# Performance work log

Measured on AMD Instinct MI355X. Metric: run time of the kernel, lower is better.

## Reference

```python
import jax, jax.numpy as jnp
import numpy as np

B, S, D = 4, 1024, 768
H = 12
E = 4
DF = 3072
TOPK = 2
# expert domain map: language->0 (LINGUISTIC), logic->1 (SYMBOLIC), spatial->0, causal->1
DOMAIN_MAP = jnp.array([0, 1, 0, 1], dtype=jnp.int32)


def layernorm(x, g, b, eps=1e-5):
    mu = jnp.mean(x, axis=-1, keepdims=True)
    var = jnp.mean(jnp.square(x - mu), axis=-1, keepdims=True)
    return (x - mu) * jax.lax.rsqrt(var + eps) * g + b


def setup_inputs() -> dict:
    key = jax.random.key(0)
    ks = jax.random.split(key, 10)
    sc = 0.02
    return {
        "x": jax.random.normal(ks[0], (B, S, D), jnp.float32),
        "ln1_g": jnp.ones((D,), jnp.float32),
        "ln1_b": jnp.zeros((D,), jnp.float32),
        "Wq": jax.random.normal(ks[1], (D, D), jnp.float32) * sc,
        "Wk": jax.random.normal(ks[2], (D, D), jnp.float32) * sc,
        "Wv": jax.random.normal(ks[3], (D, D), jnp.float32) * sc,
        "Wo": jax.random.normal(ks[4], (D, D), jnp.float32) * sc,
        "Wt": jax.random.normal(ks[5], (D, 2), jnp.float32) * sc,
        "bt": jnp.zeros((2,), jnp.float32),
        "ln2_g": jnp.ones((D,), jnp.float32),
        "ln2_b": jnp.zeros((D,), jnp.float32),
        "Wg": jax.random.normal(ks[6], (D, E), jnp.float32) * sc,
        "W1": jax.random.normal(ks[7], (E, D, DF), jnp.float32) * sc,
        "b1": jnp.zeros((E, DF), jnp.float32),
        "W2": jax.random.normal(ks[8], (E, DF, D), jnp.float32) * sc,
        "b2": jnp.zeros((E, D), jnp.float32),
    }


def reference(x, ln1_g, ln1_b, Wq, Wk, Wv, Wo, Wt, bt, ln2_g, ln2_b, Wg, W1, b1, W2, b2):
    hd = D // H
    # --- task-conditioned routing bias ---
    pooled = jnp.mean(x, axis=1)                      # [B, D]
    task_logits = pooled @ Wt + bt                    # [B, 2]
    routing_bias = task_logits[:, DOMAIN_MAP]         # [B, E]
    # --- multi-head self-attention with pre-norm residual ---
    h = layernorm(x, ln1_g, ln1_b)
    q = (h @ Wq).reshape(B, S, H, hd)
    k = (h @ Wk).reshape(B, S, H, hd)
    v = (h @ Wv).reshape(B, S, H, hd)
    scores = jnp.einsum("bqhd,bkhd->bhqk", q, k) / jnp.sqrt(jnp.float32(hd))
    attn = jax.nn.softmax(scores, axis=-1)
    ctx = jnp.einsum("bhqk,bkhd->bqhd", attn, v).reshape(B, S, D)
    x = x + ctx @ Wo
    # --- top-k MoE with routing bias, pre-norm residual ---
    h2 = layernorm(x, ln2_g, ln2_b)
    gate_logits = h2 @ Wg + routing_bias[:, None, :]  # [B, S, E]
    topv, topi = jax.lax.top_k(gate_logits, TOPK)     # [B, S, k]
    w = jax.nn.softmax(topv, axis=-1)                 # renormalized top-k weights
    gates = jnp.sum(jax.nn.one_hot(topi, E, dtype=x.dtype) * w[..., None], axis=-2)  # [B,S,E]
    hid = jax.nn.gelu(jnp.einsum("bsd,edf->bsef", h2, W1) + b1)       # [B,S,E,DF]
    y = jnp.einsum("bsef,efd->bsed", hid, W2) + b2                    # [B,S,E,D]
    moe_out = jnp.einsum("bsed,bse->bsd", y, gates)
    return x + moe_out
```

## Files before the change

kernel.cpp:

```cpp
#include <hip/hip_runtime.h>
#include <hip/hip_bf16.h>

using bf16 = __hip_bfloat16;
typedef float f32x4 __attribute__((ext_vector_type(4)));
typedef short bf16x8 __attribute__((ext_vector_type(8)));

#define DD 768
#define SS 1024
#define HH 12
#define DFF 3072

__device__ __forceinline__ float bf2f(bf16 v) { return __bfloat162float(v); }
__device__ __forceinline__ bf16 f2bf(float v) { return __float2bfloat16(v); }
__device__ __forceinline__ float sb2f(short u) {
  return __uint_as_float(((unsigned)(unsigned short)u) << 16);
}
__device__ __forceinline__ short f2sb(float f) {
  bf16 b = f2bf(f);
  return reinterpret_cast<short&>(b);
}

__device__ __forceinline__ void gld16(const void* g, void* l) {
  __builtin_amdgcn_global_load_lds(
      (const __attribute__((address_space(1))) void*)g,
      (__attribute__((address_space(3))) void*)l, 16, 0, 0);
}

__global__ __launch_bounds__(256) void transpose_cast_kernel(
    const float* __restrict__ src, bf16* __restrict__ dst,
    int R, int C, long sstride, long dstride)
{
  __shared__ float tile[64][65];
  const int c0 = blockIdx.x * 64, r0 = blockIdx.y * 64;
  const float* s = src + (long)blockIdx.z * sstride + (long)r0 * C + c0;
  bf16* d = dst + (long)blockIdx.z * dstride + (long)c0 * R + r0;
  const int rr = threadIdx.x >> 4;
  const int cc = (threadIdx.x & 15) * 4;
  #pragma unroll
  for (int k = 0; k < 4; k++) {
    const f32x4 v = *(const f32x4*)(s + (long)(rr + k * 16) * C + cc);
    *(f32x4*)(&tile[rr + k * 16][cc]) = v;
  }
  __syncthreads();
  #pragma unroll
  for (int k = 0; k < 4; k++) {
    const int c = rr + k * 16;
    short4 pk = make_short4(f2sb(tile[cc + 0][c]), f2sb(tile[cc + 1][c]),
                            f2sb(tile[cc + 2][c]), f2sb(tile[cc + 3][c]));
    *(short4*)(d + (long)c * R + cc) = pk;
  }
}

__global__ __launch_bounds__(256) void transpose4_kernel(
    const float* __restrict__ s0, const float* __restrict__ s1,
    const float* __restrict__ s2, const float* __restrict__ s3,
    bf16* __restrict__ dst)
{
  __shared__ float tile[64][65];
  const int z = blockIdx.z;
  const float* src = (z == 0) ? s0 : (z == 1) ? s1 : (z == 2) ? s2 : s3;
  const int c0 = blockIdx.x * 64, r0 = blockIdx.y * 64;
  const float* s = src + (long)r0 * 768 + c0;
  bf16* d = dst + (long)z * 589824 + (long)c0 * 768 + r0;
  const int rr = threadIdx.x >> 4;
  const int cc = (threadIdx.x & 15) * 4;
  #pragma unroll
  for (int k = 0; k < 4; k++) {
    const f32x4 v = *(const f32x4*)(s + (long)(rr + k * 16) * 768 + cc);
    *(f32x4*)(&tile[rr + k * 16][cc]) = v;
  }
  __syncthreads();
  #pragma unroll
  for (int k = 0; k < 4; k++) {
    const int c = rr + k * 16;
    short4 pk = make_short4(f2sb(tile[cc + 0][c]), f2sb(tile[cc + 1][c]),
                            f2sb(tile[cc + 2][c]), f2sb(tile[cc + 3][c]));
    *(short4*)(d + (long)c * 768 + cc) = pk;
  }
}

__global__ __launch_bounds__(256) void ln1pool_kernel(
    const float* __restrict__ x, const float* __restrict__ g,
    const float* __restrict__ b, bf16* __restrict__ out,
    float* __restrict__ pp)
{
  __shared__ float buf[4][768];
  const int w = threadIdx.x >> 6, lane = threadIdx.x & 63;
  const int row = blockIdx.x * 4 + w;
  const float* xr = x + (long)row * DD;
  float v[12];
  float s = 0.f;
  #pragma unroll
  for (int i = 0; i < 12; i++) { v[i] = xr[lane + i * 64]; s += v[i]; }
  #pragma unroll
  for (int o = 1; o < 64; o <<= 1) s += __shfl_xor(s, o, 64);
  const float mu = s * (1.f / DD);
  float vs = 0.f;
  #pragma unroll
  for (int i = 0; i < 12; i++) { const float d = v[i] - mu; vs += d * d; }
  #pragma unroll
  for (int o = 1; o < 64; o <<= 1) vs += __shfl_xor(vs, o, 64);
  const float rstd = rsqrtf(vs * (1.f / DD) + 1e-5f);
  bf16* orow = out + (long)row * DD;
  #pragma unroll
  for (int i = 0; i < 12; i++) {
    const int d = lane + i * 64;
    orow[d] = f2bf((v[i] - mu) * rstd * g[d] + b[d]);
    buf[w][d] = v[i];
  }
  __syncthreads();
  for (int c = threadIdx.x; c < 768; c += 256)
    pp[(long)blockIdx.x * 768 + c] = buf[0][c] + buf[1][c] + buf[2][c] + buf[3][c];
}

__global__ __launch_bounds__(256) void pool2_kernel(
    const float* __restrict__ pp, float* __restrict__ pooled)
{
  const int idx = blockIdx.x * 256 + threadIdx.x;
  const int bb = idx / 768, d = idx % 768;
  const float* p = pp + (long)bb * 256 * 768 + d;
  float s = 0.f;
  for (int c = 0; c < 256; c++) s += p[(long)c * 768];
  pooled[idx] = s * (1.f / SS);
}

__global__ __launch_bounds__(256) void route_kernel(
    const float* __restrict__ pooled, const float* __restrict__ Wt,
    const float* __restrict__ bt, float* __restrict__ rbias)
{
  __shared__ float tl[8];
  const int pair = threadIdx.x >> 5, l = threadIdx.x & 31;
  const int b = pair >> 1, j = pair & 1;
  float s = 0.f;
  for (int i = l; i < DD; i += 32) s += pooled[b * DD + i] * Wt[i * 2 + j];
  #pragma unroll
  for (int o = 1; o < 32; o <<= 1) s += __shfl_xor(s, o, 64);
  if (l == 0) tl[pair] = s + bt[j];
  __syncthreads();
  if (threadIdx.x < 16) {
    const int bb = threadIdx.x >> 2, e = threadIdx.x & 3;
    rbias[threadIdx.x] = tl[bb * 2 + (e & 1)];
  }
}

__device__ __forceinline__ float gelu_tanh(float x) {
  const float u = 0.7978845608028654f * (x + 0.044715f * x * x * x);
  const float e = __expf(2.f * u);
  const float t = 1.f - 2.f / (e + 1.f);
  return 0.5f * x * (1.f + t);
}

template <int MODE>
__global__ __launch_bounds__(256) void gemm128_kernel(
    const bf16* __restrict__ A, const bf16* __restrict__ Bt,
    bf16* __restrict__ Cbf, float* __restrict__ Cf,
    int N, int K, int NT, int GX,
    const float* __restrict__ aux1)
{
  __shared__ __align__(16) bf16 As[2][128 * 32];
  __shared__ __align__(16) bf16 Bs[2][128 * 32];

  const int nwg = gridDim.x;
  const int orig = blockIdx.x;
  const int q = nwg >> 3, r = nwg & 7;
  const int xcd = orig & 7, sidx = orig >> 3;
  const int wgid = (xcd < r ? xcd * (q + 1) : r * (q + 1) + (xcd - r) * q) + sidx;

  const int n0 = (wgid % GX) * 128;
  const int m0 = (wgid / GX) * 128;

  const int tid = threadIdx.x;
  const int lane = tid & 63, wv = tid >> 6;
  const int wr = wv >> 1, wc = wv & 1;
  const int lrow = lane & 15, lk = lane >> 4;
  const int lr = lrow, lg = lk;
  const int srow = lane >> 2;
  const int csw = (((lane & 3) ^ ((srow >> 1) & 3)) * 8);

  const bf16* arow[2];
  const bf16* brow[2];
  #pragma unroll
  for (int u = 0; u < 2; u++) {
    const int rbr = u * 64 + wv * 16 + srow;
    arow[u] = A + (long)(m0 + rbr) * K;
    brow[u] = Bt + (long)(n0 + rbr) * K;
  }

  f32x4 acc[4][4] = {};

#define STAGE(T, BUF)                                                   \
  {                                                                     \
    const int k0s = (T) * 32;                                           \
    _Pragma("unroll")                                                   \
    for (int u = 0; u < 2; u++) {                                       \
      const int rb = u * 64 + wv * 16;                                  \
      gld16(arow[u] + k0s + csw, &As[BUF][rb * 32]);                    \
      gld16(brow[u] + k0s + csw, &Bs[BUF][rb * 32]);                    \
    }                                                                   \
  }

  STAGE(0, 0)
  __syncthreads();

  for (int t = 0; t < NT; t++) {
    const int buf = t & 1;
    if (t + 1 < NT) STAGE(t + 1, buf ^ 1)

    bf16x8 af[4], bfr[4];
    #pragma unroll
    for (int i = 0; i < 4; i++) {
      const int ra = wr * 64 + i * 16 + lrow;
      const int rbw = wc * 64 + i * 16 + lrow;
      af[i]  = *(const bf16x8*)(&As[buf][ra * 32 + ((lk ^ ((ra >> 1) & 3)) * 8)]);
      bfr[i] = *(const bf16x8*)(&Bs[buf][rbw * 32 + ((lk ^ ((rbw >> 1) & 3)) * 8)]);
    }
    #pragma unroll
    for (int i = 0; i < 4; i++)
      #pragma unroll
      for (int j = 0; j < 4; j++)
        acc[i][j] = __builtin_amdgcn_mfma_f32_16x16x32_bf16(bfr[j], af[i], acc[i][j], 0, 0, 0);
    __syncthreads();
  }
#undef STAGE

  #pragma unroll
  for (int i = 0; i < 4; i++) {
    const int rloc = wr * 64 + i * 16 + lr;
    #pragma unroll
    for (int j = 0; j < 4; j++) {
      const int col = n0 + wc * 64 + j * 16 + lg * 4;
      const f32x4 v = acc[i][j];
      if (MODE == 0) {
        const long row = m0 + rloc;
        short4 pk = make_short4(f2sb(v[0]), f2sb(v[1]), f2sb(v[2]), f2sb(v[3]));
        *(short4*)(&Cbf[row * N + col]) = pk;
      } else {
        const long idx = (long)(m0 + rloc) * N + col;
        const f32x4 xv = *(const f32x4*)(&aux1[idx]);
        f32x4 o = xv + v;
        *(f32x4*)(&Cf[idx]) = o;
      }
    }
  }
}

template <int MODE>
__global__ __launch_bounds__(512, 2) void gemm256s_kernel(
    const bf16* __restrict__ A, const bf16* __restrict__ Bt,
    bf16* __restrict__ Cbf,
    int N, int K, int NT, int GX,
    const float* __restrict__ aux1, const float* __restrict__ gates,
    const int* __restrict__ tokl, const int* __restrict__ cnt_es,
    bf16* __restrict__ yB)
{
  __shared__ __align__(16) bf16 As[2][256 * 32];
  __shared__ __align__(16) bf16 Bs[2][256 * 32];

  const int nwg = gridDim.x;
  const int orig = blockIdx.x;
  const int q = nwg >> 3, r = nwg & 7;
  const int xcd = orig & 7, sidx = orig >> 3;
  const int wgid = (xcd < r ? xcd * (q + 1) : r * (q + 1) + (xcd - r) * q) + sidx;

  const int n0 = (wgid % GX) * 256;
  int e = 0, g0 = 0, row0 = 0, nval = 0, kseg = 0, kh = 0;
  {
    int p = wgid / GX;
    if (MODE == 3) { kh = p & 1; p >>= 1; }
    int sacc = 0, pacc = 0, found = 0;
    #pragma unroll
    for (int k = 0; k < 8; k++) {
      const int c = cnt_es[k];
      const int pk = (c + 255) >> 8;
      if (!found && p < pacc + pk) {
        found = 1; kseg = k; e = k & 3;
        g0 = (p - pacc) * 256; row0 = sacc + g0; nval = c;
      }
      pacc += pk; sacc += c;
    }
    if (!found) return;
  }
  const int kofs = (MODE == 3) ? kh * 1536 : 0;

  const int tid = threadIdx.x;
  const int lane = tid & 63, wv = tid >> 6;
  const int wr = wv >> 2, wc = wv & 3;
  const int lrow = lane & 15, lk = lane >> 4;
  const int lr = lrow, lg = lk;
  const int srow = lane >> 2;
  const int csw = (((lane & 3) ^ ((srow >> 1) & 3)) * 8);

  const bf16* Be = Bt + (long)e * N * K;
  const bf16* arow[2];
  const bf16* brow[2];
  #pragma unroll
  for (int u = 0; u < 2; u++) {
    const int rbr = u * 128 + wv * 16 + srow;
    if (MODE == 2) {
      const int g = g0 + rbr;
      const int tk = (g < nval) ? tokl[kseg * 4096 + g] : tokl[kseg * 4096];
      arow[u] = A + (long)tk * K;
    } else {
      int rr = row0 + rbr; if (rr > 8191) rr = 8191;
      arow[u] = A + (long)rr * K + kofs;
    }
    brow[u] = Be + (long)(n0 + rbr) * K + kofs;
  }

  f32x4 acc[8][4] = {};

#define STAGE(T, BUF)                                                   \
  {                                                                     \
    const int k0s = (T) * 32;                                           \
    _Pragma("unroll")                                                   \
    for (int u = 0; u < 2; u++) {                                       \
      const int rb = u * 128 + wv * 16;                                 \
      gld16(arow[u] + k0s + csw, &As[BUF][rb * 32]);                    \
      gld16(brow[u] + k0s + csw, &Bs[BUF][rb * 32]);                    \
    }                                                                   \
  }

  STAGE(0, 0)
  __syncthreads();

  for (int t = 0; t < NT; t++) {
    const int buf = t & 1;
    if (t + 1 < NT) STAGE(t + 1, buf ^ 1)

    bf16x8 af[8], bfr[4];
    #pragma unroll
    for (int j = 0; j < 4; j++) {
      const int rbw = wc * 64 + j * 16 + lrow;
      bfr[j] = *(const bf16x8*)(&Bs[buf][rbw * 32 + ((lk ^ ((rbw >> 1) & 3)) * 8)]);
    }
    #pragma unroll
    for (int i = 0; i < 8; i++) {
      const int ra = wr * 128 + i * 16 + lrow;
      af[i] = *(const bf16x8*)(&As[buf][ra * 32 + ((lk ^ ((ra >> 1) & 3)) * 8)]);
    }
    #pragma unroll
    for (int i = 0; i < 8; i++)
      #pragma unroll
      for (int j = 0; j < 4; j++)
        acc[i][j] = __builtin_amdgcn_mfma_f32_16x16x32_bf16(bfr[j], af[i], acc[i][j], 0, 0, 0);
    __syncthreads();
  }
#undef STAGE

  #pragma unroll
  for (int i = 0; i < 8; i++) {
    const int g = g0 + wr * 128 + i * 16 + lr;
    if (g < nval) {
      #pragma unroll
      for (int j = 0; j < 4; j++) {
        const int col = n0 + wc * 64 + j * 16 + lg * 4;
        const f32x4 v = acc[i][j];
        if (MODE == 2) {
          const float* b1e = aux1 + (long)e * N;
          const f32x4 bb = *(const f32x4*)(&b1e[col]);
          short4 pk = make_short4(f2sb(gelu_tanh(v[0] + bb[0])),
                                  f2sb(gelu_tanh(v[1] + bb[1])),
                                  f2sb(gelu_tanh(v[2] + bb[2])),
                                  f2sb(gelu_tanh(v[3] + bb[3])));
          *(short4*)(&Cbf[(long)(row0 - g0 + g) * N + col]) = pk;
        } else {
          const int tk = tokl[kseg * 4096 + g];
          const float gt = gates[tk * 4 + e];
          f32x4 vb = v;
          if (kh == 0) {
            const float* b2e = aux1 + (long)e * N;
            const f32x4 bb = *(const f32x4*)(&b2e[col]);
            vb = v + bb;
          }
          const int pidx = (kseg >> 2) * 2 + kh;
          bf16* yp = (pidx < 3) ? Cbf + (long)pidx * 3145728 : yB;
          short4 pk = make_short4(f2sb(gt * vb[0]), f2sb(gt * vb[1]),
                                  f2sb(gt * vb[2]), f2sb(gt * vb[3]));
          *(short4*)(&yp[(long)tk * 768 + col]) = pk;
        }
      }
    }
  }
}

__global__ __launch_bounds__(256) void fuse_kernel(
    const bf16* __restrict__ yA, const bf16* __restrict__ yB,
    float* __restrict__ out)
{
  const long i = ((long)blockIdx.x * 256 + threadIdx.x) * 4;
  const short4 a = *(const short4*)((const short*)yA + i);
  const short4 b = *(const short4*)((const short*)yA + 3145728 + i);
  const short4 c = *(const short4*)((const short*)yA + 6291456 + i);
  const short4 d = *(const short4*)((const short*)yB + i);
  f32x4 o = *(f32x4*)(&out[i]);
  o[0] += sb2f(a.x) + sb2f(b.x) + sb2f(c.x) + sb2f(d.x);
  o[1] += sb2f(a.y) + sb2f(b.y) + sb2f(c.y) + sb2f(d.y);
  o[2] += sb2f(a.z) + sb2f(b.z) + sb2f(c.z) + sb2f(d.z);
  o[3] += sb2f(a.w) + sb2f(b.w) + sb2f(c.w) + sb2f(d.w);
  *(f32x4*)(&out[i]) = o;
}

__global__ __launch_bounds__(256) void vtrans_kernel(
    const bf16* __restrict__ qkv, bf16* __restrict__ vt)
{
  __shared__ short t[64][72];
  const int kt = blockIdx.x;
  const int bh = blockIdx.y;
  const int b = bh / HH, h = bh % HH;
  const int tid = threadIdx.x;
  const short* vg = (const short*)qkv + ((long)(b * SS + kt * 64)) * 2304 + 1536 + h * 64;
  #pragma unroll
  for (int i = 0; i < 2; i++) {
    const int idx = i * 256 + tid;
    const int r = idx >> 3, c = (idx & 7) * 8;
    *(bf16x8*)(&t[r][c]) = *(const bf16x8*)(vg + (long)r * 2304 + c);
  }
  __syncthreads();
  short* vo = (short*)vt + (long)bh * 64 * SS + kt * 64;
  #pragma unroll
  for (int i = 0; i < 2; i++) {
    const int idx = i * 256 + tid;
    const int d = idx >> 3, r0 = (idx & 7) * 8;
    bf16x8 o;
    #pragma unroll
    for (int j = 0; j < 8; j++) o[j] = t[r0 + j][d];
    *(bf16x8*)(vo + (long)d * SS + r0) = o;
  }
}

__global__ __launch_bounds__(256) void attn_kernel(
    const bf16* __restrict__ qkv, const bf16* __restrict__ vt,
    bf16* __restrict__ ctx)
{
  __shared__ __align__(16) short Qs[64 * 64];
  __shared__ __align__(16) short Ks[64 * 64];
  __shared__ __align__(16) short Vts[64 * 64];
  __shared__ __align__(16) short Ps[4][16 * 64];

  const int qt = blockIdx.x;
  const int bh = blockIdx.y;
  const int b = bh / HH, h = bh % HH;
  const int tid = threadIdx.x, lane = tid & 63, w = tid >> 6;
  const int lr = lane & 15, lg = lane >> 4;

  const short* qg = (const short*)qkv + ((long)(b * SS + qt * 64)) * 2304 + h * 64;
  #pragma unroll
  for (int i = 0; i < 2; i++) {
    const int idx = i * 256 + tid;
    const int r = idx >> 3, c8 = idx & 7;
    bf16x8 v = *(const bf16x8*)(qg + (long)r * 2304 + c8 * 8);
    bf16x8 o;
    #pragma unroll
    for (int j = 0; j < 8; j++) o[j] = f2sb(sb2f(v[j]) * 0.125f);
    *(bf16x8*)(&Qs[r * 64 + ((c8 ^ (r & 7)) * 8)]) = o;
  }
  __syncthreads();

  bf16x8 aq[2];
  {
    const int r = w * 16 + lr;
    aq[0] = *(const bf16x8*)(&Qs[r * 64 + (((lg + 0) ^ (r & 7)) * 8)]);
    aq[1] = *(const bf16x8*)(&Qs[r * 64 + (((lg + 4) ^ (r & 7)) * 8)]);
  }

  float m_run[4], l_run[4];
  f32x4 oacc[4];
  #pragma unroll
  for (int r = 0; r < 4; r++) { m_run[r] = -1e30f; l_run[r] = 0.f; }
  #pragma unroll
  for (int dt = 0; dt < 4; dt++) oacc[dt] = (f32x4){0.f, 0.f, 0.f, 0.f};

  const short* kg = (const short*)qkv + ((long)(b * SS)) * 2304 + 768 + h * 64;
  const short* vg = (const short*)vt + ((long)bh * 64) * SS;
  const int sr = lane >> 3, sc = lane & 7;

  for (int kt = 0; kt < 16; kt++) {
    __syncthreads();
    #pragma unroll
    for (int c = 0; c < 2; c++) {
      const int rb = c * 32 + w * 8;
      const int row = rb + sr;
      const int ch = sc ^ (row & 7);
      gld16(kg + ((long)(kt * 64 + row)) * 2304 + ch * 8, &Ks[rb * 64]);
      gld16(vg + ((long)row) * SS + kt * 64 + ch * 8, &Vts[rb * 64]);
    }
    __syncthreads();

    f32x4 s[4];
    #pragma unroll
    for (int jt = 0; jt < 4; jt++) {
      const int r = jt * 16 + lr;
      bf16x8 bk0 = *(const bf16x8*)(&Ks[r * 64 + (((lg + 0) ^ (r & 7)) * 8)]);
      bf16x8 bk1 = *(const bf16x8*)(&Ks[r * 64 + (((lg + 4) ^ (r & 7)) * 8)]);
      f32x4 a = {};
      a = __builtin_amdgcn_mfma_f32_16x16x32_bf16(aq[0], bk0, a, 0, 0, 0);
      a = __builtin_amdgcn_mfma_f32_16x16x32_bf16(aq[1], bk1, a, 0, 0, 0);
      s[jt] = a;
    }

    #pragma unroll
    for (int r = 0; r < 4; r++) {
      float mt = fmaxf(fmaxf(s[0][r], s[1][r]), fmaxf(s[2][r], s[3][r]));
      mt = fmaxf(mt, __shfl_xor(mt, 1, 64));
      mt = fmaxf(mt, __shfl_xor(mt, 2, 64));
      mt = fmaxf(mt, __shfl_xor(mt, 4, 64));
      mt = fmaxf(mt, __shfl_xor(mt, 8, 64));
      const float mn = fmaxf(m_run[r], mt);
      const float sc0 = __expf(m_run[r] - mn);
      m_run[r] = mn;
      float p0 = __expf(s[0][r] - mn), p1 = __expf(s[1][r] - mn);
      float p2 = __expf(s[2][r] - mn), p3 = __expf(s[3][r] - mn);
      float rs = p0 + p1 + p2 + p3;
      rs += __shfl_xor(rs, 1, 64);
      rs += __shfl_xor(rs, 2, 64);
      rs += __shfl_xor(rs, 4, 64);
      rs += __shfl_xor(rs, 8, 64);
      l_run[r] = l_run[r] * sc0 + rs;
      #pragma unroll
      for (int dt = 0; dt < 4; dt++) oacc[dt][r] *= sc0;
      const int prow = lg * 4 + r;
      const int pswz = (prow & 7) << 3;
      Ps[w][prow * 64 + ((0 * 16 + lr) ^ pswz)] = f2sb(p0);
      Ps[w][prow * 64 + ((1 * 16 + lr) ^ pswz)] = f2sb(p1);
      Ps[w][prow * 64 + ((2 * 16 + lr) ^ pswz)] = f2sb(p2);
      Ps[w][prow * 64 + ((3 * 16 + lr) ^ pswz)] = f2sb(p3);
    }

    bf16x8 pa0 = *(const bf16x8*)(&Ps[w][lr * 64 + (((lg + 0) ^ (lr & 7)) << 3)]);
    bf16x8 pa1 = *(const bf16x8*)(&Ps[w][lr * 64 + (((lg + 4) ^ (lr & 7)) << 3)]);
    #pragma unroll
    for (int dt = 0; dt < 4; dt++) {
      const int r = dt * 16 + lr;
      bf16x8 bv0 = *(const bf16x8*)(&Vts[r * 64 + (((lg + 0) ^ (r & 7)) * 8)]);
      bf16x8 bv1 = *(const bf16x8*)(&Vts[r * 64 + (((lg + 4) ^ (r & 7)) * 8)]);
      oacc[dt] = __builtin_amdgcn_mfma_f32_16x16x32_bf16(pa0, bv0, oacc[dt], 0, 0, 0);
      oacc[dt] = __builtin_amdgcn_mfma_f32_16x16x32_bf16(pa1, bv1, oacc[dt], 0, 0, 0);
    }
  }

  #pragma unroll
  for (int r = 0; r < 4; r++) {
    const float inv = 1.f / l_run[r];
    const long row = (long)(b * SS + qt * 64 + w * 16 + lg * 4 + r);
    #pragma unroll
    for (int dt = 0; dt < 4; dt++)
      ctx[row * DD + h * 64 + dt * 16 + lr] = f2bf(oacc[dt][r] * inv);
  }
}

__global__ __launch_bounds__(256) void lngate_kernel(
    const float* __restrict__ x2, const float* __restrict__ g,
    const float* __restrict__ bln, const float* __restrict__ Wg,
    const float* __restrict__ rbias, bf16* __restrict__ h2,
    float* __restrict__ gates)
{
  const int t = blockIdx.x * 4 + (threadIdx.x >> 6);
  const int lane = threadIdx.x & 63;
  const int b = t >> 10;
  const float* xr = x2 + (long)t * DD;
  float v[12];
  float s = 0.f;
  #pragma unroll
  for (int i = 0; i < 12; i++) { v[i] = xr[lane + i * 64]; s += v[i]; }
  #pragma unroll
  for (int o = 1; o < 64; o <<= 1) s += __shfl_xor(s, o, 64);
  const float mu = s * (1.f / DD);
  float vs = 0.f;
  #pragma unroll
  for (int i = 0; i < 12; i++) { const float d = v[i] - mu; vs += d * d; }
  #pragma unroll
  for (int o = 1; o < 64; o <<= 1) vs += __shfl_xor(vs, o, 64);
  const float rstd = rsqrtf(vs * (1.f / DD) + 1e-5f);
  bf16* orow = h2 + (long)t * DD;
  float a0 = 0.f, a1 = 0.f, a2 = 0.f, a3 = 0.f;
  #pragma unroll
  for (int i = 0; i < 12; i++) {
    const int d = lane + i * 64;
    const float hv = (v[i] - mu) * rstd * g[d] + bln[d];
    orow[d] = f2bf(hv);
    const f32x4 w = *(const f32x4*)(&Wg[d * 4]);
    a0 += hv * w.x; a1 += hv * w.y; a2 += hv * w.z; a3 += hv * w.w;
  }
  #pragma unroll
  for (int o = 1; o < 64; o <<= 1) {
    a0 += __shfl_xor(a0, o, 64); a1 += __shfl_xor(a1, o, 64);
    a2 += __shfl_xor(a2, o, 64); a3 += __shfl_xor(a3, o, 64);
  }
  if (lane == 0) {
    float lg4[4] = { a0 + rbias[b * 4 + 0], a1 + rbias[b * 4 + 1],
                     a2 + rbias[b * 4 + 2], a3 + rbias[b * 4 + 3] };
    int i1 = 0;
    #pragma unroll
    for (int e = 1; e < 4; e++) if (lg4[e] > lg4[i1]) i1 = e;
    int i2 = -1;
    #pragma unroll
    for (int e = 0; e < 4; e++) if (e != i1 && (i2 < 0 || lg4[e] > lg4[i2])) i2 = e;
    const float e2 = __expf(lg4[i2] - lg4[i1]);
    const float den = 1.f + e2;
    float og[4] = {0.f, 0.f, 0.f, 0.f};
    og[i1] = 1.f / den;
    og[i2] = e2 / den;
    *(f32x4*)(&gates[t * 4]) = (f32x4){og[0], og[1], og[2], og[3]};
  }
}

__global__ __launch_bounds__(1024) void compact_kernel(
    const float* __restrict__ gates, int* __restrict__ tokl,
    int* __restrict__ cnt)
{
  __shared__ int wtot[8][16];
  const int tid = threadIdx.x;
  const int lane = tid & 63, w = tid >> 6;
  int sA[4], sB[4];
  int lc[8] = {0, 0, 0, 0, 0, 0, 0, 0};
  #pragma unroll
  for (int i = 0; i < 4; i++) {
    const int t = tid * 4 + i;
    const f32x4 g = *(const f32x4*)(&gates[t * 4]);
    int e1 = -1, e2 = -1;
    #pragma unroll
    for (int e = 0; e < 4; e++)
      if (g[e] > 0.f) { if (e1 < 0) e1 = e; else e2 = e; }
    sA[i] = e1; sB[i] = 4 + e2;
    lc[e1]++; lc[4 + e2]++;
  }
  int base[8];
  #pragma unroll
  for (int k = 0; k < 8; k++) {
    int v = lc[k];
    #pragma unroll
    for (int o = 1; o < 64; o <<= 1) {
      const int u = __shfl_up(v, o, 64);
      if (lane >= o) v += u;
    }
    base[k] = v - lc[k];
    if (lane == 63) wtot[k][w] = v;
  }
  __syncthreads();
  #pragma unroll
  for (int k = 0; k < 8; k++) {
    int b = 0;
    for (int ww = 0; ww < 16; ww++)
      if (ww < w) b += wtot[k][ww];
    base[k] += b;
  }
  #pragma unroll
  for (int i = 0; i < 4; i++) {
    const int t = tid * 4 + i;
    tokl[sA[i] * 4096 + base[sA[i]]] = t; base[sA[i]]++;
    tokl[sB[i] * 4096 + base[sB[i]]] = t; base[sB[i]]++;
  }
  if (tid < 8) {
    int s = 0;
    for (int ww = 0; ww < 16; ww++) s += wtot[tid][ww];
    cnt[tid] = s;
  }
}

extern "C" void kernel_launch(void* const* d_in, const int* in_sizes, int n_in,
                              void* d_out, int out_size, void* d_ws, size_t ws_size,
                              hipStream_t stream)
{
  (void)in_sizes; (void)n_in; (void)out_size; (void)ws_size;
  const float* x    = (const float*)d_in[0];
  const float* ln1g = (const float*)d_in[1];
  const float* ln1b = (const float*)d_in[2];
  const float* Wq   = (const float*)d_in[3];
  const float* Wk   = (const float*)d_in[4];
  const float* Wv   = (const float*)d_in[5];
  const float* Wo   = (const float*)d_in[6];
  const float* Wt   = (const float*)d_in[7];
  const float* bt   = (const float*)d_in[8];
  const float* ln2g = (const float*)d_in[9];
  const float* ln2b = (const float*)d_in[10];
  const float* Wg   = (const float*)d_in[11];
  const float* W1   = (const float*)d_in[12];
  const float* b1   = (const float*)d_in[13];
  const float* W2   = (const float*)d_in[14];
  const float* b2   = (const float*)d_in[15];
  float* out = (float*)d_out;

  char* ws = (char*)d_ws;
  bf16*  w1t    = (bf16*)(ws + 0);
  bf16*  w2t    = (bf16*)(ws + 18874368);
  bf16*  h2     = (bf16*)(ws + 37748736);
  float* gates  = (float*)(ws + 44040192);
  int*   tokl   = (int*)(ws + 44105728);
  int*   cnt    = (int*)(ws + 44236800);
  float* pooled = (float*)(ws + 44237056);
  float* rbias  = (float*)(ws + 44249344);
  bf16*  wqkv_t = (bf16*)(ws + 44249600);
  bf16*  h1     = (bf16*)(ws + 48968192);
  bf16*  qkv    = (bf16*)(ws + 55259648);
  bf16*  ctx    = (bf16*)(ws + 74134016);
  bf16*  hid    = (bf16*)(ws + 44249600);
  bf16*  wo_t   = wqkv_t + 3 * 589824;
  bf16*  vt     = h1;
  bf16*  yA     = w1t;
  bf16*  yB     = h2;
  float* pp     = (float*)qkv;

  transpose4_kernel<<<dim3(12, 12, 4), 256, 0, stream>>>(Wq, Wk, Wv, Wo, wqkv_t);
  transpose_cast_kernel<<<dim3(48, 12, 4), 256, 0, stream>>>(W1, w1t, 768, 3072, 2359296, 2359296);
  transpose_cast_kernel<<<dim3(12, 48, 4), 256, 0, stream>>>(W2, w2t, 3072, 768, 2359296, 2359296);

  ln1pool_kernel<<<1024, 256, 0, stream>>>(x, ln1g, ln1b, h1, pp);
  pool2_kernel<<<12, 256, 0, stream>>>(pp, pooled);
  route_kernel<<<1, 256, 0, stream>>>(pooled, Wt, bt, rbias);

  gemm128_kernel<0><<<32 * 18, 256, 0, stream>>>(h1, wqkv_t, qkv, nullptr,
                                                 2304, 768, 24, 18, nullptr);
  vtrans_kernel<<<dim3(16, 48), 256, 0, stream>>>(qkv, vt);
  attn_kernel<<<dim3(16, 48), 256, 0, stream>>>(qkv, vt, ctx);
  gemm128_kernel<1><<<32 * 6, 256, 0, stream>>>(ctx, wo_t, nullptr, out,
                                                768, 768, 24, 6, x);
  lngate_kernel<<<1024, 256, 0, stream>>>(out, ln2g, ln2b, Wg, rbias, h2, gates);
  compact_kernel<<<1, 1024, 0, stream>>>(gates, tokl, cnt);

  gemm256s_kernel<2><<<40 * 12, 512, 0, stream>>>(h2, w1t, hid,
                                                  3072, 768, 24, 12,
                                                  b1, nullptr, tokl, cnt, nullptr);
  gemm256s_kernel<3><<<40 * 2 * 3, 512, 0, stream>>>(hid, w2t, yA,
                                                     768, 3072, 48, 3,
                                                     b2, gates, tokl, cnt, yB);
  fuse_kernel<<<3072, 256, 0, stream>>>(yA, yB, out);
}
```

Baseline: 322.6 us.

## Triple-buffer LDS in 256-tile GEMM with split staging and explicit waitcnt

Moves the 256x256 expert GEMM kernel from double to triple buffered LDS, prefetching two K-tiles ahead. The A and B global-to-LDS loads are split across two MFMA phases, with s_waitcnt vmcnt replacing the full __syncthreads, plus s_setprio around the MFMA bursts. The goal is to hide global load latency and barrier stalls. The larger LDS footprint (96KB) and dropping the min-2-blocks launch bound may reduce occupancy, and the manual vmcnt counting has to match the load counts exactly.

```diff
diff --git a/kernel.cpp b/kernel.cpp
--- a/kernel.cpp
+++ b/kernel.cpp
@@ -245,7 +245,7 @@
 }
 
 template <int MODE>
-__global__ __launch_bounds__(512, 2) void gemm256s_kernel(
+__global__ __launch_bounds__(512) void gemm256s_kernel(
     const bf16* __restrict__ A, const bf16* __restrict__ Bt,
     bf16* __restrict__ Cbf,
     int N, int K, int NT, int GX,
@@ -253,8 +253,8 @@
     const int* __restrict__ tokl, const int* __restrict__ cnt_es,
     bf16* __restrict__ yB)
 {
-  __shared__ __align__(16) bf16 As[2][256 * 32];
-  __shared__ __align__(16) bf16 Bs[2][256 * 32];
+  __shared__ __align__(16) bf16 As[3][256 * 32];
+  __shared__ __align__(16) bf16 Bs[3][256 * 32];
 
   const int nwg = gridDim.x;
   const int orig = blockIdx.x;
@@ -309,43 +309,82 @@
 
   f32x4 acc[8][4] = {};
 
-#define STAGE(T, BUF)                                                   \
+#define STAGE_A(T, BUF)                                                 \
   {                                                                     \
     const int k0s = (T) * 32;                                           \
     _Pragma("unroll")                                                   \
     for (int u = 0; u < 2; u++) {                                       \
       const int rb = u * 128 + wv * 16;                                 \
       gld16(arow[u] + k0s + csw, &As[BUF][rb * 32]);                    \
+    }                                                                   \
+  }
+#define STAGE_B(T, BUF)                                                 \
+  {                                                                     \
+    const int k0s = (T) * 32;                                           \
+    _Pragma("unroll")                                                   \
+    for (int u = 0; u < 2; u++) {                                       \
+      const int rb = u * 128 + wv * 16;                                 \
       gld16(brow[u] + k0s + csw, &Bs[BUF][rb * 32]);                    \
     }                                                                   \
   }
 
-  STAGE(0, 0)
-  __syncthreads();
+  STAGE_A(0, 0) STAGE_B(0, 0)
+  STAGE_A(1, 1) STAGE_B(1, 1)
+  asm volatile("s_waitcnt vmcnt(4)" ::: "memory");
+  __builtin_amdgcn_s_barrier();
+  __builtin_amdgcn_sched_barrier(0);
 
   for (int t = 0; t < NT; t++) {
-    const int buf = t & 1;
-    if (t + 1 < NT) STAGE(t + 1, buf ^ 1)
-
-    bf16x8 af[8], bfr[4];
+    const int buf = t % 3;
+    const int nbuf = (t + 2) % 3;
+
+    if (t + 2 < NT) STAGE_A(t + 2, nbuf)
+    bf16x8 bfr[4], af[4];
     #pragma unroll
     for (int j = 0; j < 4; j++) {
       const int rbw = wc * 64 + j * 16 + lrow;
       bfr[j] = *(const bf16x8*)(&Bs[buf][rbw * 32 + ((lk ^ ((rbw >> 1) & 3)) * 8)]);
     }
     #pragma unroll
-    for (int i = 0; i < 8; i++) {
+    for (int i = 0; i < 4; i++) {
       const int ra = wr * 128 + i * 16 + lrow;
       af[i] = *(const bf16x8*)(&As[buf][ra * 32 + ((lk ^ ((ra >> 1) & 3)) * 8)]);
     }
-    #pragma unroll
-    for (int i = 0; i < 8; i++)
+    asm volatile("s_waitcnt lgkmcnt(0)" ::: "memory");
+    __builtin_amdgcn_sched_barrier(0);
+    __builtin_amdgcn_s_setprio(1);
+    #pragma unroll
+    for (int i = 0; i < 4; i++)
       #pragma unroll
       for (int j = 0; j < 4; j++)
         acc[i][j] = __builtin_amdgcn_mfma_f32_16x16x32_bf16(bfr[j], af[i], acc[i][j], 0, 0, 0);
-    __syncthreads();
-  }
-#undef STAGE
+    __builtin_amdgcn_s_setprio(0);
+    __builtin_amdgcn_sched_barrier(0);
+
+    if (t + 2 < NT) STAGE_B(t + 2, nbuf)
+    #pragma unroll
+    for (int i = 0; i < 4; i++) {
+      const int ra = wr * 128 + (i + 4) * 16 + lrow;
+      af[i] = *(const bf16x8*)(&As[buf][ra * 32 + ((lk ^ ((ra >> 1) & 3)) * 8)]);
+    }
+    asm volatile("s_waitcnt lgkmcnt(0)" ::: "memory");
+    __builtin_amdgcn_sched_barrier(0);
+    __builtin_amdgcn_s_setprio(1);
+    #pragma unroll
+    for (int i = 0; i < 4; i++)
+      #pragma unroll
+      for (int j = 0; j < 4; j++)
+        acc[i + 4][j] = __builtin_amdgcn_mfma_f32_16x16x32_bf16(bfr[j], af[i], acc[i + 4][j], 0, 0, 0);
+    __builtin_amdgcn_s_setprio(0);
+    __builtin_amdgcn_sched_barrier(0);
+
+    if (t + 2 < NT) asm volatile("s_waitcnt vmcnt(4)" ::: "memory");
+    else            asm volatile("s_waitcnt vmcnt(0)" ::: "memory");
+    __builtin_amdgcn_s_barrier();
+    __builtin_amdgcn_sched_barrier(0);
+  }
+#undef STAGE_A
+#undef STAGE_B
 
   #pragma unroll
   for (int i = 0; i < 8; i++) {
```

After: 328.7 us. No clear change (+1.9%).

## Rewrite MoE expert GEMM mainloop with 64-wide K tiles and phased prefetch

Applied to the files above, without the earlier changes.

The routed MoE expert GEMMs now use 64-wide K tiles in shared memory with an XOR swizzle, which halves the number of K iterations. The main loop is split into four phases that interleave staged global-to-LDS loads with MFMA work. A ping-pong schedule prefetches A one tile ahead and B two tiles ahead, using explicit vmcnt/lgkmcnt waits, raw s_barrier and priority boosts around the MFMA blocks. LDS use doubles to 128 KB, so occupancy drops to one workgroup per CU, and the hand-written wait counts add risk of subtle synchronisation errors.

```diff
diff --git a/kernel.cpp b/kernel.cpp
--- a/kernel.cpp
+++ b/kernel.cpp
@@ -245,7 +245,7 @@
 }
 
 template <int MODE>
-__global__ __launch_bounds__(512, 2) void gemm256s_kernel(
+__global__ __launch_bounds__(512, 1) void gemm256p_kernel(
     const bf16* __restrict__ A, const bf16* __restrict__ Bt,
     bf16* __restrict__ Cbf,
     int N, int K, int NT, int GX,
@@ -253,8 +253,8 @@
     const int* __restrict__ tokl, const int* __restrict__ cnt_es,
     bf16* __restrict__ yB)
 {
-  __shared__ __align__(16) bf16 As[2][256 * 32];
-  __shared__ __align__(16) bf16 Bs[2][256 * 32];
+  __shared__ __align__(16) bf16 Al[2][256 * 64];
+  __shared__ __align__(16) bf16 Bl[2][256 * 64];
 
   const int nwg = gridDim.x;
   const int orig = blockIdx.x;
@@ -287,65 +287,108 @@
   const int wr = wv >> 2, wc = wv & 3;
   const int lrow = lane & 15, lk = lane >> 4;
   const int lr = lrow, lg = lk;
-  const int srow = lane >> 2;
-  const int csw = (((lane & 3) ^ ((srow >> 1) & 3)) * 8);
+
+  const int strow = tid >> 3;
+  const int stch = tid & 7;
+  const int ssw = ((stch ^ (strow & 7)) * 8);
 
   const bf16* Be = Bt + (long)e * N * K;
-  const bf16* arow[2];
-  const bf16* brow[2];
-  #pragma unroll
-  for (int u = 0; u < 2; u++) {
-    const int rbr = u * 128 + wv * 16 + srow;
-    if (MODE == 2) {
-      const int g = g0 + rbr;
-      const int tk = (g < nval) ? tokl[kseg * 4096 + g] : tokl[kseg * 4096];
-      arow[u] = A + (long)tk * K;
-    } else {
-      int rr = row0 + rbr; if (rr > 8191) rr = 8191;
-      arow[u] = A + (long)rr * K + kofs;
-    }
-    brow[u] = Be + (long)(n0 + rbr) * K + kofs;
+  const bf16* pA[2][2];
+  const bf16* pB[2][2];
+  #pragma unroll
+  for (int h = 0; h < 2; h++)
+    #pragma unroll
+    for (int c = 0; c < 2; c++) {
+      const int rt = h * 128 + c * 64 + strow;
+      if (MODE == 2) {
+        const int g = g0 + rt;
+        const int tk = (g < nval) ? tokl[kseg * 4096 + g] : tokl[kseg * 4096];
+        pA[h][c] = A + (long)tk * K + kofs + ssw;
+      } else {
+        int rr = row0 + rt; if (rr > 8191) rr = 8191;
+        pA[h][c] = A + (long)rr * K + kofs + ssw;
+      }
+      pB[h][c] = Be + (long)(n0 + rt) * K + kofs + ssw;
+    }
+
+#define LDSA(BUF, H, C) (&Al[BUF][(((H) * 128 + (C) * 64 + wv * 8)) * 64])
+#define LDSB(BUF, H, C) (&Bl[BUF][(((H) * 128 + (C) * 64 + wv * 8)) * 64])
+#define SGA(H, KT, BUF) { gld16(pA[H][0] + (KT) * 64, LDSA(BUF, H, 0)); \
+                          gld16(pA[H][1] + (KT) * 64, LDSA(BUF, H, 1)); }
+#define SGB(H, KT, BUF) { gld16(pB[H][0] + (KT) * 64, LDSB(BUF, H, 0)); \
+                          gld16(pB[H][1] + (KT) * 64, LDSB(BUF, H, 1)); }
+
+  int aoff[2], boff[2];
+  #pragma unroll
+  for (int ks = 0; ks < 2; ks++) {
+    aoff[ks] = (wr * 128 + lrow) * 64 + (((ks * 4 + lk) ^ (lrow & 7)) * 8);
+    boff[ks] = (wc * 64 + lrow) * 64 + (((ks * 4 + lk) ^ (lrow & 7)) * 8);
   }
 
   f32x4 acc[8][4] = {};
 
-#define STAGE(T, BUF)                                                   \
-  {                                                                     \
-    const int k0s = (T) * 32;                                           \
-    _Pragma("unroll")                                                   \
-    for (int u = 0; u < 2; u++) {                                       \
-      const int rb = u * 128 + wv * 16;                                 \
-      gld16(arow[u] + k0s + csw, &As[BUF][rb * 32]);                    \
-      gld16(brow[u] + k0s + csw, &Bs[BUF][rb * 32]);                    \
-    }                                                                   \
-  }
-
-  STAGE(0, 0)
-  __syncthreads();
-
-  for (int t = 0; t < NT; t++) {
-    const int buf = t & 1;
-    if (t + 1 < NT) STAGE(t + 1, buf ^ 1)
-
-    bf16x8 af[8], bfr[4];
-    #pragma unroll
-    for (int j = 0; j < 4; j++) {
-      const int rbw = wc * 64 + j * 16 + lrow;
-      bfr[j] = *(const bf16x8*)(&Bs[buf][rbw * 32 + ((lk ^ ((rbw >> 1) & 3)) * 8)]);
-    }
-    #pragma unroll
-    for (int i = 0; i < 8; i++) {
-      const int ra = wr * 128 + i * 16 + lrow;
-      af[i] = *(const bf16x8*)(&As[buf][ra * 32 + ((lk ^ ((ra >> 1) & 3)) * 8)]);
-    }
-    #pragma unroll
-    for (int i = 0; i < 8; i++)
+  SGA(0, 0, 0) SGA(1, 0, 0)
+  SGB(0, 0, 0) SGB(1, 0, 0)
+  SGB(0, 1, 1) SGB(1, 1, 1)
+  asm volatile("s_waitcnt vmcnt(4)" ::: "memory");
+  __builtin_amdgcn_s_barrier();
+  __builtin_amdgcn_sched_barrier(0);
+
+  bf16x8 bfr[4][2];
+
+  for (int kt = 0; kt < NT; kt++) {
+    const int buf = kt & 1;
+    const int ao = buf * 16384, bo = buf * 16384;
+    const bool stA = (kt + 1 < NT);
+    const bool stB = (kt + 2 < NT);
+
+    #pragma unroll
+    for (int ph = 0; ph < 4; ph++) {
+      if (ph == 0) { if (stA) SGA(0, kt + 1, buf ^ 1) }
+      else if (ph == 1) { if (stA) SGA(1, kt + 1, buf ^ 1) }
+      else if (ph == 2) { if (stB) SGB(0, kt + 2, buf) }
+      else { if (stB) SGB(1, kt + 2, buf) }
+
+      bf16x8 af[2][2];
+      if (ph == 0) {
+        #pragma unroll
+        for (int j = 0; j < 4; j++)
+          #pragma unroll
+          for (int ks = 0; ks < 2; ks++)
+            bfr[j][ks] = *(const bf16x8*)(&Bl[0][bo + boff[ks] + j * 1024]);
+      }
       #pragma unroll
-      for (int j = 0; j < 4; j++)
-        acc[i][j] = __builtin_amdgcn_mfma_f32_16x16x32_bf16(bfr[j], af[i], acc[i][j], 0, 0, 0);
-    __syncthreads();
-  }
-#undef STAGE
+      for (int i2 = 0; i2 < 2; i2++)
+        #pragma unroll
+        for (int ks = 0; ks < 2; ks++)
+          af[i2][ks] = *(const bf16x8*)(&Al[0][ao + aoff[ks] + (ph * 2 + i2) * 1024]);
+
+      asm volatile("s_waitcnt lgkmcnt(0)" ::: "memory");
+      __builtin_amdgcn_sched_barrier(0);
+      __builtin_amdgcn_s_setprio(1);
+      #pragma unroll
+      for (int i2 = 0; i2 < 2; i2++)
+        #pragma unroll
+        for (int j = 0; j < 4; j++)
+          #pragma unroll
+          for (int ks = 0; ks < 2; ks++)
+            acc[ph * 2 + i2][j] = __builtin_amdgcn_mfma_f32_16x16x32_bf16(
+                bfr[j][ks], af[i2][ks], acc[ph * 2 + i2][j], 0, 0, 0);
+      __builtin_amdgcn_s_setprio(0);
+      __builtin_amdgcn_sched_barrier(0);
+
+      if (ph == 3) {
+        if (stB) asm volatile("s_waitcnt vmcnt(4)" ::: "memory");
+        else     asm volatile("s_waitcnt vmcnt(0)" ::: "memory");
+      }
+      __builtin_amdgcn_s_barrier();
+      __builtin_amdgcn_sched_barrier(0);
+    }
+  }
+#undef SGA
+#undef SGB
+#undef LDSA
+#undef LDSB
 
   #pragma unroll
   for (int i = 0; i < 8; i++) {
@@ -717,11 +760,11 @@
   lngate_kernel<<<1024, 256, 0, stream>>>(out, ln2g, ln2b, Wg, rbias, h2, gates);
   compact_kernel<<<1, 1024, 0, stream>>>(gates, tokl, cnt);
 
-  gemm256s_kernel<2><<<40 * 12, 512, 0, stream>>>(h2, w1t, hid,
-                                                  3072, 768, 24, 12,
+  gemm256p_kernel<2><<<40 * 12, 512, 0, stream>>>(h2, w1t, hid,
+                                                  3072, 768, 12, 12,
                                                   b1, nullptr, tokl, cnt, nullptr);
-  gemm256s_kernel<3><<<40 * 2 * 3, 512, 0, stream>>>(hid, w2t, yA,
-                                                     768, 3072, 48, 3,
+  gemm256p_kernel<3><<<40 * 2 * 3, 512, 0, stream>>>(hid, w2t, yA,
+                                                     768, 3072, 24, 3,
                                                      b2, gates, tokl, cnt, yB);
   fuse_kernel<<<3072, 256, 0, stream>>>(yA, yB, out);
 }
```

Measured after the change: 321.6 us. Within noise of the previous version (-0.3%).
